# Kernel tuning notes

Measured on AMD Instinct MI355X. Metric: run time of the kernel, lower is better.

The kernel has to match this reference:

```python
import jax, jax.numpy as jnp
import numpy as np

_MEAN = jnp.array([0.485, 0.456, 0.406], dtype=jnp.float32)
_STD = jnp.array([0.229, 0.224, 0.225], dtype=jnp.float32)
_EPS = 1e-8


def _conv_relu(x, w, b):
    # VGG conv: 3x3, stride 1, pad 1, followed by ReLU. x: [B,C,H,W], w: [O,I,3,3]
    y = jax.lax.conv_general_dilated(x, w, (1, 1), 'SAME',
                                     dimension_numbers=('NCHW', 'OIHW', 'NCHW'))
    return jax.nn.relu(y + b[None, :, None, None])


def _maxpool2(x):
    return jax.lax.reduce_window(x, -jnp.inf, jax.lax.max,
                                 (1, 1, 2, 2), (1, 1, 2, 2), 'VALID')


def _vgg_block3_feats(x, w0, b0, w1, b1, w2, b2, w3, b3, w4, b4, w5, b5, w6, b6):
    # Replicates VGG16.features up to index 15, collecting relu outputs at 11,13,15.
    x = (x - _MEAN[None, :, None, None]) / _STD[None, :, None, None]
    x = _conv_relu(x, w0, b0)            # conv1_1 (idx 0,1)
    x = _conv_relu(x, w1, b1)            # conv1_2 (idx 2,3)
    x = _maxpool2(x)                     # idx 4
    x = _conv_relu(x, w2, b2)            # conv2_1 (idx 5,6)
    x = _conv_relu(x, w3, b3)            # conv2_2 (idx 7,8)
    x = _maxpool2(x)                     # idx 9
    f1 = _conv_relu(x, w4, b4)           # relu after conv3_1 -> idx 11
    f2 = _conv_relu(f1, w5, b5)          # relu after conv3_2 -> idx 13
    f3 = _conv_relu(f2, w6, b6)          # relu after conv3_3 -> idx 15
    # torch.cat([...], dim=1)
    return jnp.concatenate([f1, f2, f3], axis=1)  # [B, 768, H/4, W/4]


def _feat_replace_and_cos_loss(x_feats, s_feats):
    # x_feats, s_feats: [B, C, h, w]. All-pairs cosine NN match across spatial locations.
    B, C, h, w = x_feats.shape
    x_flat = x_feats.reshape(B, C, h * w).transpose(0, 2, 1)   # [B, N, C]
    s_flat = s_feats.reshape(B, C, -1).transpose(0, 2, 1)       # [B, M, C]
    xn = x_flat / (jnp.linalg.norm(x_flat, axis=-1, keepdims=True) + _EPS)
    sn = s_flat / (jnp.linalg.norm(s_flat, axis=-1, keepdims=True) + _EPS)
    sim = jnp.einsum('bnc,bmc->bnm', xn, sn)                    # [B, N, M] (dominant intermediate)
    idx = jnp.argmax(sim, axis=-1)                              # nearest style feature per location
    target = jnp.take_along_axis(s_flat, idx[..., None], axis=1)  # [B, N, C]
    target = jax.lax.stop_gradient(target)                      # styles are under no_grad
    tn = target / (jnp.linalg.norm(target, axis=-1, keepdims=True) + _EPS)
    cos_d = jnp.sum(xn * tn, axis=-1)                           # cosine sim along channel dim
    return jnp.mean(1.0 - cos_d)


def setup_inputs() -> dict:
    key = jax.random.key(0)
    ks = jax.random.split(key, 16)
    outputs = jax.random.uniform(ks[0], (4, 3, 256, 256), dtype=jnp.float32)
    styles = jax.random.uniform(ks[1], (4, 3, 256, 256), dtype=jnp.float32)
    # VGG16 conv stack up to conv3_3 (OIHW), He-scaled random weights
    chans = [(64, 3), (64, 64), (128, 64), (128, 128), (256, 128), (256, 256), (256, 256)]
    inp = {'outputs': outputs, 'styles': styles}
    for i, (o, c) in enumerate(chans):
        std = float(np.sqrt(2.0 / (c * 9)))
        inp[f'w{i}'] = jax.random.normal(ks[2 + 2 * i], (o, c, 3, 3), dtype=jnp.float32) * std
        inp[f'b{i}'] = jnp.zeros((o,), dtype=jnp.float32)
    return inp


def reference(outputs, styles, w0, b0, w1, b1, w2, b2, w3, b3, w4, b4, w5, b5, w6, b6):
    params = (w0, b0, w1, b1, w2, b2, w3, b3, w4, b4, w5, b5, w6, b6)
    x_feats = _vgg_block3_feats(outputs, *params)
    s_feats = jax.lax.stop_gradient(_vgg_block3_feats(styles, *params))  # with torch.no_grad()
    nn_loss = _feat_replace_and_cos_loss(x_feats, s_feats)
    return nn_loss
```

## Files before the change

### kernel.cpp

```cpp
#include <hip/hip_runtime.h>
#include <hip/hip_bf16.h>

__constant__ float c_mean[3] = {0.485f, 0.456f, 0.406f};
__constant__ float c_istd[3] = {1.0f/0.229f, 1.0f/0.224f, 1.0f/0.225f};

typedef __attribute__((ext_vector_type(8))) short short8;
typedef __attribute__((ext_vector_type(4))) float floatv4;
typedef unsigned short ushort;

__device__ inline float bf2f(ushort u) {
  unsigned int x = ((unsigned int)u) << 16;
  float f; __builtin_memcpy(&f, &x, 4); return f;
}
__device__ inline ushort f2bf(float f) {
  __hip_bfloat16 h = __float2bfloat16(f);
  ushort u; __builtin_memcpy(&u, &h, 2); return u;
}

__global__ __launch_bounds__(256) void zero_k(float* __restrict__ p, int n)
{
  int i = blockIdx.x * 256 + threadIdx.x;
  if (i < n) p[i] = 0.f;
}

__global__ __launch_bounds__(256) void wtrans_k(const float* __restrict__ w,
                                                ushort* __restrict__ Wp,
                                                int OC, int IC)
{
  int t = blockIdx.x * 256 + threadIdx.x;
  int total = OC * IC * 9;
  if (t >= total) return;
  int oct16 = OC >> 4;
  int j = t & 7;
  int L = (t >> 3) & 63;
  int f = t >> 9;
  int ot = f % oct16;
  int r  = f / oct16;
  int tap = r % 9;
  int kc  = r / 9;
  int oc = ot * 16 + (L & 15);
  int ic = kc * 32 + ((L >> 4) << 3) + j;
  float v = w[((size_t)oc * IC + ic) * 9 + tap];
  ushort h = f2bf(v);
  Wp[(size_t)f * 1024 + L * 8 + j]       = h;
  Wp[(size_t)f * 1024 + 512 + L * 8 + j] = f2bf(v - bf2f(h));
}

__global__ __launch_bounds__(256) void conv0_k(const float* __restrict__ imgA,
                                               const float* __restrict__ imgB,
                                               const float* __restrict__ w,
                                               const float* __restrict__ bias,
                                               ushort* __restrict__ Yh)
{
  __shared__ float wl[27][64];
  __shared__ float bl[64];
  const int tid = threadIdx.x;
  for (int i = tid; i < 1728; i += 256) {
    int o = i & 63, t = i >> 6;
    wl[t][o] = w[o * 27 + t];
  }
  if (tid < 64) bl[tid] = bias[tid];
  __syncthreads();
  int px = blockIdx.x * 256 + tid;
  int b = px >> 16, rem = px & 65535;
  int y = rem >> 8, x = rem & 255;
  const float* img = (b < 4) ? (imgA + (size_t)b * 3 * 65536)
                             : (imgB + (size_t)(b - 4) * 3 * 65536);
  float iv[27];
#pragma unroll
  for (int c = 0; c < 3; ++c)
#pragma unroll
    for (int dy = 0; dy < 3; ++dy)
#pragma unroll
      for (int dx = 0; dx < 3; ++dx) {
        int gy = y - 1 + dy, gx = x - 1 + dx;
        float v = 0.f;
        if (gy >= 0 && gy < 256 && gx >= 0 && gx < 256)
          v = (img[(size_t)c * 65536 + gy * 256 + gx] - c_mean[c]) * c_istd[c];
        iv[c * 9 + dy * 3 + dx] = v;
      }
  float acc[64];
#pragma unroll
  for (int o = 0; o < 64; ++o) acc[o] = 0.f;
#pragma unroll
  for (int t = 0; t < 27; ++t) {
    float v = iv[t];
#pragma unroll
    for (int o = 0; o < 64; ++o) acc[o] = fmaf(v, wl[t][o], acc[o]);
  }
  size_t base = (size_t)px * 64;
#pragma unroll
  for (int o8 = 0; o8 < 8; ++o8) {
    short8 vh;
#pragma unroll
    for (int j = 0; j < 8; ++j)
      vh[j] = (short)f2bf(fmaxf(acc[o8 * 8 + j] + bl[o8 * 8 + j], 0.f));
    *(short8*)(Yh + base + o8 * 8) = vh;
  }
}

template<int TH, int WPY, int WPO, bool POOL, bool SSQ>
__global__ __launch_bounds__(256) void convmf_k(
    const ushort* __restrict__ Xh,
    const ushort* __restrict__ Wp,
    const float* __restrict__ bias,
    ushort* __restrict__ Yh,
    float* __restrict__ ssq,
    int H, int W, int IC, int in_stride, int ic_off,
    int OC, int out_stride, int oc_off, int octiles)
{
  constexpr int HR = TH + 2;
  constexpr int HALO = HR * 18;
  constexpr int OCB = WPO * 64;
  __shared__ ushort xs_h[4 * HALO * 8];

  const int tid = threadIdx.x;
  const int wave = tid >> 6, lane = tid & 63;
  const int quad = lane >> 4, l16 = lane & 15;
  const int wy = wave / WPO, wo = wave % WPO;
  const int bb = blockIdx.z / octiles, ot = blockIdx.z % octiles;
  const int y0 = blockIdx.y * TH, x0 = blockIdx.x * 16;
  const int ocbase = ot * OCB + wo * 64;
  const int oct16 = OC >> 4;

  floatv4 acc[4][4];
#pragma unroll
  for (int tn = 0; tn < 4; ++tn)
#pragma unroll
    for (int tm = 0; tm < 4; ++tm) acc[tn][tm] = (floatv4){0.f, 0.f, 0.f, 0.f};

  for (int k0 = 0; k0 < IC; k0 += 32) {
    __syncthreads();
    for (int u = tid; u < HALO * 4; u += 256) {
      int px = u >> 2, icq = u & 3;
      int hy = px / 18, hx = px - hy * 18;
      int gy = y0 - 1 + hy, gx = x0 - 1 + hx;
      int4 vh = {0, 0, 0, 0};
      if (gy >= 0 && gy < H && gx >= 0 && gx < W) {
        size_t g = ((size_t)(bb * H + gy) * W + gx) * in_stride + ic_off + k0 + icq * 8;
        vh = *(const int4*)(Xh + g);
      }
      *(int4*)&xs_h[(icq * HALO + px) * 8] = vh;
    }
    __syncthreads();

#pragma unroll
    for (int tap = 0; tap < 9; ++tap) {
      const int dy = tap / 3, dx = tap % 3;
      const size_t wg = (((size_t)(k0 >> 5) * 9 + tap) * oct16 + (ocbase >> 4)) * 1024 + (size_t)lane * 8;
      short8 bh[4], bl4[4];
#pragma unroll
      for (int tm = 0; tm < 4; ++tm) {
        bh[tm]  = *(const short8*)(Wp + wg + tm * 1024);
        bl4[tm] = *(const short8*)(Wp + wg + tm * 1024 + 512);
      }
#pragma unroll
      for (int tn = 0; tn < 4; ++tn) {
        int p = wy * 64 + tn * 16 + l16;
        int ty = p >> 4, tx = p & 15;
        int hp = (ty + dy) * 18 + tx + dx;
        short8 ah = *(const short8*)&xs_h[(quad * HALO + hp) * 8];
#pragma unroll
        for (int tm = 0; tm < 4; ++tm) {
          acc[tn][tm] = __builtin_amdgcn_mfma_f32_16x16x32_bf16(ah, bh[tm],  acc[tn][tm], 0, 0, 0);
          acc[tn][tm] = __builtin_amdgcn_mfma_f32_16x16x32_bf16(ah, bl4[tm], acc[tn][tm], 0, 0, 0);
        }
      }
    }
  }

  if (POOL) {
    const int oH = H >> 1, oW = W >> 1;
#pragma unroll
    for (int tm = 0; tm < 4; ++tm) {
      int ocg = ocbase + tm * 16 + l16;
      float bv = bias[ocg];
#pragma unroll
      for (int tn2 = 0; tn2 < 2; ++tn2)
#pragma unroll
        for (int r2 = 0; r2 < 2; ++r2) {
          float v0 = fmaxf(acc[2 * tn2][tm][2 * r2]     + bv, 0.f);
          float v1 = fmaxf(acc[2 * tn2][tm][2 * r2 + 1] + bv, 0.f);
          float v2 = fmaxf(acc[2 * tn2 + 1][tm][2 * r2]     + bv, 0.f);
          float v3 = fmaxf(acc[2 * tn2 + 1][tm][2 * r2 + 1] + bv, 0.f);
          float v = fmaxf(fmaxf(v0, v1), fmaxf(v2, v3));
          int oy = (y0 >> 1) + wy * 2 + tn2;
          int ox = (x0 >> 1) + quad * 2 + r2;
          Yh[((size_t)(bb * oH + oy) * oW + ox) * out_stride + oc_off + ocg] = f2bf(v);
        }
    }
  } else {
    float sv[4][4];
    if (SSQ) {
#pragma unroll
      for (int tn = 0; tn < 4; ++tn)
#pragma unroll
        for (int r = 0; r < 4; ++r) sv[tn][r] = 0.f;
    }
#pragma unroll
    for (int tm = 0; tm < 4; ++tm) {
      int ocg = ocbase + tm * 16 + l16;
      float bv = bias[ocg];
#pragma unroll
      for (int tn = 0; tn < 4; ++tn)
#pragma unroll
        for (int r = 0; r < 4; ++r) {
          int p = wy * 64 + tn * 16 + quad * 4 + r;
          int ty = p >> 4, tx = p & 15;
          float v = fmaxf(acc[tn][tm][r] + bv, 0.f);
          ushort h = f2bf(v);
          if (SSQ) { float vr = bf2f(h); sv[tn][r] = fmaf(vr, vr, sv[tn][r]); }
          Yh[((size_t)(bb * H + y0 + ty) * W + x0 + tx) * out_stride + oc_off + ocg] = h;
        }
    }
    if (SSQ) {
#pragma unroll
      for (int tn = 0; tn < 4; ++tn)
#pragma unroll
        for (int r = 0; r < 4; ++r) {
          float s = sv[tn][r];
          s += __shfl_xor(s, 1, 64);
          s += __shfl_xor(s, 2, 64);
          s += __shfl_xor(s, 4, 64);
          s += __shfl_xor(s, 8, 64);
          if (l16 == 0) {
            int p = wy * 64 + tn * 16 + quad * 4 + r;
            int ty = p >> 4, tx = p & 15;
            atomicAdd(&ssq[(size_t)bb * 4096 + (y0 + ty) * 64 + x0 + tx], s);
          }
        }
    }
  }
}

__global__ __launch_bounds__(256) void finalize_k(float* __restrict__ p, int n)
{
  int i = blockIdx.x * 256 + threadIdx.x;
  if (i < n) p[i] = 1.0f / (sqrtf(p[i]) + 1e-8f);
}

__global__ __launch_bounds__(256) void simmax_k(
    const ushort* __restrict__ Ch,
    const float* __restrict__ invns, float* __restrict__ partial)
{
  __shared__ ushort xh[128][72];
  __shared__ ushort sh[128][72];
  __shared__ float redbuf[2][128];
  const int tid = threadIdx.x;
  const int lane = tid & 63, wave = tid >> 6;
  const int quad = lane >> 4, l16 = lane & 15;
  const int wn0 = (wave >> 1) * 64;
  const int wm0 = (wave & 1) * 64;
  const int n0 = blockIdx.x * 128;
  const int ms = blockIdx.y;
  const int b  = blockIdx.z;

  const int row  = tid >> 1;
  const int half = tid & 1;

  float runmax[4][4];
#pragma unroll
  for (int tn = 0; tn < 4; ++tn)
#pragma unroll
    for (int r = 0; r < 4; ++r) runmax[tn][r] = -1e30f;

  const size_t xbase = ((size_t)b * 4096 + n0) * 768;

  for (int mc = 0; mc < 4; ++mc) {
    const int m0 = ms * 512 + mc * 128;
    const size_t sbase = ((size_t)(b + 4) * 4096 + m0) * 768;
    floatv4 acc[4][4];
#pragma unroll
    for (int tn = 0; tn < 4; ++tn)
#pragma unroll
      for (int tm = 0; tm < 4; ++tm) acc[tn][tm] = (floatv4){0.f, 0.f, 0.f, 0.f};

    for (int k0 = 0; k0 < 768; k0 += 64) {
      __syncthreads();
      const ushort* gx = Ch + xbase + (size_t)row * 768 + k0 + half * 32;
      const ushort* gs = Ch + sbase + (size_t)row * 768 + k0 + half * 32;
      ushort* lx = &xh[row][half * 32];
      ushort* ls = &sh[row][half * 32];
#pragma unroll
      for (int j = 0; j < 4; ++j) {
        *(int4*)(lx + j * 8) = *(const int4*)(gx + j * 8);
        *(int4*)(ls + j * 8) = *(const int4*)(gs + j * 8);
      }
      __syncthreads();
#pragma unroll
      for (int ks = 0; ks < 2; ++ks) {
        short8 ah[4], bh[4];
#pragma unroll
        for (int t = 0; t < 4; ++t) {
          ah[t] = *(const short8*)&xh[wn0 + t * 16 + l16][ks * 32 + quad * 8];
          bh[t] = *(const short8*)&sh[wm0 + t * 16 + l16][ks * 32 + quad * 8];
        }
#pragma unroll
        for (int tn = 0; tn < 4; ++tn)
#pragma unroll
          for (int tm = 0; tm < 4; ++tm)
            acc[tn][tm] = __builtin_amdgcn_mfma_f32_16x16x32_bf16(ah[tn], bh[tm], acc[tn][tm], 0, 0, 0);
      }
    }
#pragma unroll
    for (int tm = 0; tm < 4; ++tm) {
      float inv = invns[(size_t)b * 4096 + m0 + wm0 + tm * 16 + l16];
#pragma unroll
      for (int tn = 0; tn < 4; ++tn)
#pragma unroll
        for (int r = 0; r < 4; ++r)
          runmax[tn][r] = fmaxf(runmax[tn][r], acc[tn][tm][r] * inv);
    }
  }

#pragma unroll
  for (int off = 1; off < 16; off <<= 1)
#pragma unroll
    for (int tn = 0; tn < 4; ++tn)
#pragma unroll
      for (int r = 0; r < 4; ++r)
        runmax[tn][r] = fmaxf(runmax[tn][r], __shfl_xor(runmax[tn][r], off, 64));

  if (l16 == 0) {
#pragma unroll
    for (int tn = 0; tn < 4; ++tn)
#pragma unroll
      for (int r = 0; r < 4; ++r)
        redbuf[wave & 1][wn0 + tn * 16 + quad * 4 + r] = runmax[tn][r];
  }
  __syncthreads();
  if (tid < 128) {
    float mx = fmaxf(redbuf[0][tid], redbuf[1][tid]);
    partial[((size_t)ms * 4 + b) * 4096 + n0 + tid] = mx;
  }
}

__global__ __launch_bounds__(256) void loss_k(const float* __restrict__ partial,
                                              const float* __restrict__ invnx,
                                              float* __restrict__ out)
{
  float sum = 0.f;
  for (int i = threadIdx.x; i < 16384; i += 256) {
    float mx = partial[i];
#pragma unroll
    for (int j = 1; j < 8; ++j) mx = fmaxf(mx, partial[j * 16384 + i]);
    sum += mx * invnx[i];
  }
  __shared__ float red[256];
  red[threadIdx.x] = sum;
  __syncthreads();
  for (int s = 128; s > 0; s >>= 1) {
    if (threadIdx.x < s) red[threadIdx.x] += red[threadIdx.x + s];
    __syncthreads();
  }
  if (threadIdx.x == 0) out[0] = 1.f - red[0] * (1.f / 16384.f);
}

extern "C" void kernel_launch(void* const* d_in, const int* in_sizes, int n_in,
                              void* d_out, int out_size, void* d_ws, size_t ws_size,
                              hipStream_t stream)
{
  const float* outputs = (const float*)d_in[0];
  const float* styles  = (const float*)d_in[1];
  const float* w[7]; const float* bs[7];
  for (int i = 0; i < 7; ++i) { w[i] = (const float*)d_in[2 + 2 * i]; bs[i] = (const float*)d_in[3 + 2 * i]; }

  ushort* p = (ushort*)d_ws;
  ushort* A_h = p; p += 33554432;
  ushort* B_h = p; p += 8388608;
  ushort* cat_h = p; p += 25165824;
  ushort* W1p = p; p += 73728;
  ushort* W2p = p; p += 147456;
  ushort* W3p = p; p += 294912;
  ushort* W4p = p; p += 589824;
  ushort* W5p = p; p += 1179648;
  ushort* W6p = p; p += 1179648;
  float* nrm = (float*)p;
  float* partial = nrm + 32768;

  zero_k<<<dim3(128), 256, 0, stream>>>(nrm, 32768);

  wtrans_k<<<dim3((9*64*64   + 255)/256), 256, 0, stream>>>(w[1], W1p, 64, 64);
  wtrans_k<<<dim3((9*128*64  + 255)/256), 256, 0, stream>>>(w[2], W2p, 128, 64);
  wtrans_k<<<dim3((9*128*128 + 255)/256), 256, 0, stream>>>(w[3], W3p, 128, 128);
  wtrans_k<<<dim3((9*256*128 + 255)/256), 256, 0, stream>>>(w[4], W4p, 256, 128);
  wtrans_k<<<dim3((9*256*256 + 255)/256), 256, 0, stream>>>(w[5], W5p, 256, 256);
  wtrans_k<<<dim3((9*256*256 + 255)/256), 256, 0, stream>>>(w[6], W6p, 256, 256);

  conv0_k<<<dim3(2048), 256, 0, stream>>>(outputs, styles, w[0], bs[0], A_h);
  convmf_k<16,4,1,true,false><<<dim3(16,16,8), 256, 0, stream>>>(A_h, W1p, bs[1],
      B_h, nullptr, 256,256, 64, 64,0, 64, 64,0, 1);
  convmf_k<16,4,1,false,false><<<dim3(8,8,16), 256, 0, stream>>>(B_h, W2p, bs[2],
      A_h, nullptr, 128,128, 64, 64,0, 128, 128,0, 2);
  convmf_k<16,4,1,true,false><<<dim3(8,8,16), 256, 0, stream>>>(A_h, W3p, bs[3],
      B_h, nullptr, 128,128, 128, 128,0, 128, 128,0, 2);
  convmf_k<16,4,1,false,true><<<dim3(4,4,32), 256, 0, stream>>>(B_h, W4p, bs[4],
      cat_h, nrm, 64,64, 128, 128,0, 256, 768,0, 4);
  convmf_k<16,4,1,false,true><<<dim3(4,4,32), 256, 0, stream>>>(cat_h, W5p, bs[5],
      cat_h, nrm, 64,64, 256, 768,0, 256, 768,256, 4);
  convmf_k<16,4,1,false,true><<<dim3(4,4,32), 256, 0, stream>>>(cat_h, W6p, bs[6],
      cat_h, nrm, 64,64, 256, 768,256, 256, 768,512, 4);

  finalize_k<<<dim3(128), 256, 0, stream>>>(nrm, 32768);

  simmax_k<<<dim3(32, 8, 4), 256, 0, stream>>>(cat_h, nrm + 16384, partial);
  loss_k<<<dim3(1), 256, 0, stream>>>(partial, nrm, (float*)d_out);
}
```

Baseline: 658.8 us.

## Tile concatenated features in MFMA fragment layout and load X operand directly

Conv3_x layers now write the concatenated feature tensor in a 16-pixel by 8-channel tiled layout that matches the MFMA operand fragment shape, and conv3_2/3_3 read their inputs from that layout. The similarity kernel loads the X operand straight from global memory in fragment order, skipping LDS, and stages only the style tile in LDS with a simple contiguous copy using register prefetch before the barrier. It also adds an occupancy hint to launch bounds. This removes the LDS traffic and padding for X and makes global loads contiguous, but the conv epilogue stores become more scattered and the X operand is re-read from global memory/cache for every style chunk.

```diff
diff --git a/kernel.cpp b/kernel.cpp
--- a/kernel.cpp
+++ b/kernel.cpp
@@ -99,7 +99,7 @@
   }
 }
 
-template<int TH, int WPY, int WPO, bool POOL, bool SSQ>
+template<int TH, int WPY, int WPO, bool POOL, bool SSQ, bool TIN, bool TOUT>
 __global__ __launch_bounds__(256) void convmf_k(
     const ushort* __restrict__ Xh,
     const ushort* __restrict__ Wp,
@@ -137,7 +137,14 @@
       int gy = y0 - 1 + hy, gx = x0 - 1 + hx;
       int4 vh = {0, 0, 0, 0};
       if (gy >= 0 && gy < H && gx >= 0 && gx < W) {
-        size_t g = ((size_t)(bb * H + gy) * W + gx) * in_stride + ic_off + k0 + icq * 8;
+        size_t g;
+        if (TIN) {
+          int kc = (ic_off + k0 + icq * 8) >> 3;
+          g = (((size_t)(bb * ((H * W) >> 4) + gy * (W >> 4) + (gx >> 4)) * (in_stride >> 3) + kc) << 7)
+              + ((gx & 15) << 3);
+        } else {
+          g = ((size_t)(bb * H + gy) * W + gx) * in_stride + ic_off + k0 + icq * 8;
+        }
         vh = *(const int4*)(Xh + g);
       }
       *(int4*)&xs_h[(icq * HALO + px) * 8] = vh;
@@ -210,7 +217,16 @@
           float v = fmaxf(acc[tn][tm][r] + bv, 0.f);
           ushort h = f2bf(v);
           if (SSQ) { float vr = bf2f(h); sv[tn][r] = fmaf(vr, vr, sv[tn][r]); }
-          Yh[((size_t)(bb * H + y0 + ty) * W + x0 + tx) * out_stride + oc_off + ocg] = h;
+          size_t o;
+          if (TOUT) {
+            int n_out = (y0 + ty) * W + x0 + tx;
+            int oc = oc_off + ocg;
+            o = (((size_t)(bb * ((H * W) >> 4) + (n_out >> 4)) * (out_stride >> 3) + (oc >> 3)) << 7)
+                + ((n_out & 15) << 3) + (oc & 7);
+          } else {
+            o = ((size_t)(bb * H + y0 + ty) * W + x0 + tx) * out_stride + oc_off + ocg;
+          }
+          Yh[o] = h;
         }
     }
     if (SSQ) {
@@ -239,12 +255,11 @@
   if (i < n) p[i] = 1.0f / (sqrtf(p[i]) + 1e-8f);
 }
 
-__global__ __launch_bounds__(256) void simmax_k(
-    const ushort* __restrict__ Ch,
+__global__ __launch_bounds__(256, 4) void simmax_k(
+    const ushort* __restrict__ Ct,
     const float* __restrict__ invns, float* __restrict__ partial)
 {
-  __shared__ ushort xh[128][72];
-  __shared__ ushort sh[128][72];
+  __shared__ ushort sh[8192];
   __shared__ float redbuf[2][128];
   const int tid = threadIdx.x;
   const int lane = tid & 63, wave = tid >> 6;
@@ -255,45 +270,46 @@
   const int ms = blockIdx.y;
   const int b  = blockIdx.z;
 
-  const int row  = tid >> 1;
-  const int half = tid & 1;
-
   float runmax[4][4];
 #pragma unroll
   for (int tn = 0; tn < 4; ++tn)
 #pragma unroll
     for (int r = 0; r < 4; ++r) runmax[tn][r] = -1e30f;
 
-  const size_t xbase = ((size_t)b * 4096 + n0) * 768;
+  const int xtb = b * 256 + (n0 >> 4) + (wn0 >> 4);
 
   for (int mc = 0; mc < 4; ++mc) {
-    const int m0 = ms * 512 + mc * 128;
-    const size_t sbase = ((size_t)(b + 4) * 4096 + m0) * 768;
+    const int smt = (b + 4) * 256 + ms * 32 + mc * 8;
     floatv4 acc[4][4];
 #pragma unroll
     for (int tn = 0; tn < 4; ++tn)
 #pragma unroll
       for (int tm = 0; tm < 4; ++tm) acc[tn][tm] = (floatv4){0.f, 0.f, 0.f, 0.f};
 
-    for (int k0 = 0; k0 < 768; k0 += 64) {
+    for (int kc0 = 0; kc0 < 96; kc0 += 8) {
+      int4 st[4];
+#pragma unroll
+      for (int j = 0; j < 4; ++j) {
+        int idx = tid + j * 256;
+        st[j] = *(const int4*)(Ct + (((size_t)(smt + (idx >> 7)) * 96 + kc0) << 7) + ((size_t)(idx & 127) << 3));
+      }
       __syncthreads();
-      const ushort* gx = Ch + xbase + (size_t)row * 768 + k0 + half * 32;
-      const ushort* gs = Ch + sbase + (size_t)row * 768 + k0 + half * 32;
-      ushort* lx = &xh[row][half * 32];
-      ushort* ls = &sh[row][half * 32];
 #pragma unroll
       for (int j = 0; j < 4; ++j) {
-        *(int4*)(lx + j * 8) = *(const int4*)(gx + j * 8);
-        *(int4*)(ls + j * 8) = *(const int4*)(gs + j * 8);
+        int idx = tid + j * 256;
+        *(int4*)(sh + (size_t)idx * 8) = st[j];
       }
       __syncthreads();
 #pragma unroll
       for (int ks = 0; ks < 2; ++ks) {
         short8 ah[4], bh[4];
 #pragma unroll
+        for (int t = 0; t < 4; ++t)
+          ah[t] = *(const short8*)(Ct + (((size_t)(xtb + t) * 96 + kc0 + ks * 4 + quad) << 7) + ((size_t)l16 << 3));
+#pragma unroll
         for (int t = 0; t < 4; ++t) {
-          ah[t] = *(const short8*)&xh[wn0 + t * 16 + l16][ks * 32 + quad * 8];
-          bh[t] = *(const short8*)&sh[wm0 + t * 16 + l16][ks * 32 + quad * 8];
+          int mt = (wm0 >> 4) + t;
+          bh[t] = *(const short8*)&sh[(((mt * 8 + ks * 4 + quad) * 16) + l16) * 8];
         }
 #pragma unroll
         for (int tn = 0; tn < 4; ++tn)
@@ -302,6 +318,7 @@
             acc[tn][tm] = __builtin_amdgcn_mfma_f32_16x16x32_bf16(ah[tn], bh[tm], acc[tn][tm], 0, 0, 0);
       }
     }
+    const int m0 = ms * 512 + mc * 128;
 #pragma unroll
     for (int tm = 0; tm < 4; ++tm) {
       float inv = invns[(size_t)b * 4096 + m0 + wm0 + tm * 16 + l16];
@@ -388,17 +405,17 @@
   wtrans_k<<<dim3((9*256*256 + 255)/256), 256, 0, stream>>>(w[6], W6p, 256, 256);
 
   conv0_k<<<dim3(2048), 256, 0, stream>>>(outputs, styles, w[0], bs[0], A_h);
-  convmf_k<16,4,1,true,false><<<dim3(16,16,8), 256, 0, stream>>>(A_h, W1p, bs[1],
+  convmf_k<16,4,1,true,false,false,false><<<dim3(16,16,8), 256, 0, stream>>>(A_h, W1p, bs[1],
       B_h, nullptr, 256,256, 64, 64,0, 64, 64,0, 1);
-  convmf_k<16,4,1,false,false><<<dim3(8,8,16), 256, 0, stream>>>(B_h, W2p, bs[2],
+  convmf_k<16,4,1,false,false,false,false><<<dim3(8,8,16), 256, 0, stream>>>(B_h, W2p, bs[2],
       A_h, nullptr, 128,128, 64, 64,0, 128, 128,0, 2);
-  convmf_k<16,4,1,true,false><<<dim3(8,8,16), 256, 0, stream>>>(A_h, W3p, bs[3],
+  convmf_k<16,4,1,true,false,false,false><<<dim3(8,8,16), 256, 0, stream>>>(A_h, W3p, bs[3],
       B_h, nullptr, 128,128, 128, 128,0, 128, 128,0, 2);
-  convmf_k<16,4,1,false,true><<<dim3(4,4,32), 256, 0, stream>>>(B_h, W4p, bs[4],
+  convmf_k<16,4,1,false,true,false,true><<<dim3(4,4,32), 256, 0, stream>>>(B_h, W4p, bs[4],
       cat_h, nrm, 64,64, 128, 128,0, 256, 768,0, 4);
-  convmf_k<16,4,1,false,true><<<dim3(4,4,32), 256, 0, stream>>>(cat_h, W5p, bs[5],
+  convmf_k<16,4,1,false,true,true,true><<<dim3(4,4,32), 256, 0, stream>>>(cat_h, W5p, bs[5],
       cat_h, nrm, 64,64, 256, 768,0, 256, 768,256, 4);
-  convmf_k<16,4,1,false,true><<<dim3(4,4,32), 256, 0, stream>>>(cat_h, W6p, bs[6],
+  convmf_k<16,4,1,false,true,true,true><<<dim3(4,4,32), 256, 0, stream>>>(cat_h, W6p, bs[6],
       cat_h, nrm, 64,64, 256, 768,256, 256, 768,512, 4);
 
   finalize_k<<<dim3(128), 256, 0, stream>>>(nrm, 32768);
```

After: 810.2 us. 23.0% more time.
